# Performance work log

Measured on AMD Instinct MI355X. Metric: run time of the kernel, lower is better.

The kernel has to match this reference:

```python
import jax, jax.numpy as jnp
import numpy as np

N = 100000   # nodes
E = 1600000  # edges
IN, HID, OUT = 128, 128, 64


def setup_inputs() -> dict:
    key = jax.random.key(0)
    ks = jax.random.split(key, 8)
    x = jax.random.normal(ks[0], (N, IN), dtype=jnp.float32)
    edge_index = jax.random.randint(ks[1], (2, E), 0, N, dtype=jnp.int64)
    W1 = jax.random.normal(ks[2], (IN, HID), dtype=jnp.float32) * 0.05
    b1 = jnp.zeros((HID,), dtype=jnp.float32)
    W2 = jax.random.normal(ks[3], (HID, OUT), dtype=jnp.float32) * 0.05
    b2 = jnp.zeros((OUT,), dtype=jnp.float32)
    Wd = jax.random.normal(ks[4], (OUT, IN), dtype=jnp.float32) * 0.05
    bd = jnp.zeros((IN,), dtype=jnp.float32)
    return {"x": x, "edge_index": edge_index, "W1": W1, "b1": b1,
            "W2": W2, "b2": b2, "Wd": Wd, "bd": bd}


def _gcn_conv(x, src, dst, W, b):
    # PyG GCNConv: add self-loops, symmetric normalization D^-1/2 (A+I) D^-1/2,
    # messages flow src -> dst, aggregated by sum at dst.
    h = x @ W                                   # [N, F]
    ones = jnp.ones((src.shape[0],), x.dtype)
    deg = jax.ops.segment_sum(ones, dst, num_segments=N) + 1.0  # +1 for self-loop
    dinv = jax.lax.rsqrt(deg)                   # deg^-1/2, [N]
    coef = dinv[src] * dinv[dst]                # per-edge norm
    agg = jax.ops.segment_sum(h[src] * coef[:, None], dst, num_segments=N)
    agg = agg + h * (dinv * dinv)[:, None]      # self-loop contribution
    return agg + b


def reference(x, edge_index, W1, b1, W2, b2, Wd, bd):
    src, dst = edge_index[0], edge_index[1]
    h = jax.nn.relu(_gcn_conv(x, src, dst, W1, b1))
    # dropout in eval mode -> identity
    z = _gcn_conv(h, src, dst, W2, b2)          # [N, OUT] embedding
    x_recon = z @ Wd + bd                        # [N, IN]
    return (x_recon, z)
```

## Files before the change

### kernel.cpp

```cpp
#include <hip/hip_runtime.h>
#include <hip/hip_bf16.h>
#include <hip/hip_fp16.h>


#define TPB 256
#define CAP 64

typedef float v2f __attribute__((ext_vector_type(2)));


__device__ __forceinline__ unsigned short f2bf(float f) {
    unsigned u = __float_as_uint(f);
    unsigned r = u + 0x7fffu + ((u >> 16) & 1u);
    return (unsigned short)(r >> 16);
}
__device__ __forceinline__ float bf_lo(unsigned u) { return __uint_as_float(u << 16); }
__device__ __forceinline__ float bf_hi(unsigned u) { return __uint_as_float(u & 0xffff0000u); }


__global__ void count_k(const int* __restrict__ dst, int* __restrict__ cnt, int E) {
    int e0 = (blockIdx.x * TPB + threadIdx.x) * 4;
    if (e0 + 3 < E) {
        int4 d4 = *(const int4*)&dst[e0];
        atomicAdd(&cnt[d4.x], 1);
        atomicAdd(&cnt[d4.y], 1);
        atomicAdd(&cnt[d4.z], 1);
        atomicAdd(&cnt[d4.w], 1);
    } else {
        for (int e = e0; e < E; ++e) atomicAdd(&cnt[dst[e]], 1);
    }
}

__global__ void prep_k(const int* __restrict__ cnt, float* __restrict__ dinv,
                       int* __restrict__ cursor, int N) {
    int i = blockIdx.x * TPB + threadIdx.x;
    if (i < N) {
        dinv[i]   = rsqrtf((float)cnt[i] + 1.0f);
        cursor[i] = 0;
    }
}

__global__ void fill_k(const int* __restrict__ src, const int* __restrict__ dst,
                       int* __restrict__ cursor, const float* __restrict__ dinv,
                       unsigned* __restrict__ bucket, int E) {
    int e0 = (blockIdx.x * TPB + threadIdx.x) * 4;
    if (e0 + 3 < E) {
        int4 s4 = *(const int4*)&src[e0];
        int4 d4 = *(const int4*)&dst[e0];
        int ss[4] = {s4.x, s4.y, s4.z, s4.w};
        int dd[4] = {d4.x, d4.y, d4.z, d4.w};
#pragma unroll
        for (int q = 0; q < 4; ++q) {
            float c = dinv[ss[q]] * dinv[dd[q]];
            unsigned short hb = __half_as_ushort(__float2half(c));
            unsigned entry = ((unsigned)ss[q] << 15) | (unsigned)hb;
            int r = atomicAdd(&cursor[dd[q]], 1);
            if (r < CAP) bucket[(size_t)dd[q] * CAP + r] = entry;
        }
    } else {
        for (int e = e0; e < E; ++e) {
            int s = src[e], d = dst[e];
            float c = dinv[s] * dinv[d];
            unsigned short hb = __half_as_ushort(__float2half(c));
            unsigned entry = ((unsigned)s << 15) | (unsigned)hb;
            int r = atomicAdd(&cursor[d], 1);
            if (r < CAP) bucket[(size_t)d * CAP + r] = entry;
        }
    }
}


template <int K, int C, int TN, bool BIAS, bool INBF, bool OUTBF>
__global__ __launch_bounds__(TPB) void gemm_k(const void* __restrict__ Ap,
                                              const float* __restrict__ W,
                                              const float* __restrict__ bias,
                                              void* __restrict__ outp, int N) {
    constexpr int BM  = 128;
    constexpr int TM  = 8;
    constexpr int NCT = C / TN;
    static_assert(NCT * (BM / TM) == TPB, "thread layout");

    __shared__ float Ws[K * C];
    int tid = threadIdx.x;
    for (int i = tid * 4; i < K * C; i += TPB * 4)
        *(float4*)&Ws[i] = *(const float4*)&W[i];
    __syncthreads();

    int tc = tid % NCT;
    int tr = tid / NCT;
    int c0 = tc * TN;
    int r0 = blockIdx.x * BM + tr * TM;

    float acc[TM][TN] = {};

    for (int k = 0; k < K; k += 4) {
        float4 a[TM];
        uint2  au[TM];
#pragma unroll
        for (int i = 0; i < TM; ++i) {
            int r = r0 + i;
            if (r >= N) r = N - 1;
            if (INBF)
                au[i] = *(const uint2*)((const unsigned short*)Ap + (size_t)r * K + k);
            else
                a[i] = *(const float4*)((const float*)Ap + (size_t)r * K + k);
        }
#pragma unroll
        for (int kk = 0; kk < 4; ++kk) {
            float w[TN];
#pragma unroll
            for (int j = 0; j < TN; j += 4)
                *(float4*)&w[j] = *(const float4*)&Ws[(k + kk) * C + c0 + j];
#pragma unroll
            for (int i = 0; i < TM; ++i) {
                float av;
                if (INBF) {
                    unsigned uu = (kk < 2) ? au[i].x : au[i].y;
                    av = (kk & 1) ? bf_hi(uu) : bf_lo(uu);
                } else {
                    av = ((const float*)&a[i])[kk];
                }
#pragma unroll
                for (int j = 0; j < TN; ++j) acc[i][j] += av * w[j];
            }
        }
    }

#pragma unroll
    for (int i = 0; i < TM; ++i) {
        int r = r0 + i;
        if (r >= N) continue;
        if (BIAS) {
#pragma unroll
            for (int j = 0; j < TN; ++j) acc[i][j] += bias[c0 + j];
        }
        if (OUTBF) {
            unsigned short* ob = (unsigned short*)outp + (size_t)r * C + c0;
            unsigned pk[TN / 2];
#pragma unroll
            for (int j = 0; j < TN; j += 2)
                pk[j / 2] = (unsigned)f2bf(acc[i][j]) | ((unsigned)f2bf(acc[i][j + 1]) << 16);
            if (TN == 8)      *(uint4*)ob = *(uint4*)pk;
            else if (TN == 4) *(uint2*)ob = *(uint2*)pk;
        } else {
            float* of = (float*)outp + (size_t)r * C + c0;
#pragma unroll
            for (int j = 0; j < TN; j += 4)
                *(float4*)&of[j] = *(float4*)&acc[i][j];
        }
    }
}


template <int F2, bool RELU, bool OUTBF>
__global__ __launch_bounds__(TPB) void agg_k(const unsigned* __restrict__ h,
                                             const int* __restrict__ cnt,
                                             const unsigned* __restrict__ bucket,
                                             const float* __restrict__ dinv,
                                             const float* __restrict__ bias,
                                             void* __restrict__ outp, int N) {
    constexpr int NPB = TPB / F2;
    int ln = threadIdx.x / F2;
    int f2 = threadIdx.x % F2;
    int n  = blockIdx.x * NPB + ln;
    if (n >= N) return;

    float di = dinv[n];
    unsigned us = h[(size_t)n * F2 + f2];
    float ax = bf_lo(us) * (di * di);
    float ay = bf_hi(us) * (di * di);

    int cn = cnt[n];
    if (cn > CAP) cn = CAP;
    const unsigned* bk = bucket + (size_t)n * CAP;

    int j = 0;
    for (; j + 7 < cn; j += 8) {
        unsigned e[8], v[8];
        float c[8];
#pragma unroll
        for (int q = 0; q < 8; ++q) e[q] = bk[j + q];
#pragma unroll
        for (int q = 0; q < 8; ++q) {
            int s = (int)(e[q] >> 15);
            v[q] = h[(size_t)s * F2 + f2];
            c[q] = __half2float(__ushort_as_half((unsigned short)(e[q] & 0x7fffu)));
        }
#pragma unroll
        for (int q = 0; q < 8; ++q) {
            ax += c[q] * bf_lo(v[q]);
            ay += c[q] * bf_hi(v[q]);
        }
    }
    for (; j < cn; ++j) {
        unsigned e = bk[j];
        int s = (int)(e >> 15);
        unsigned v = h[(size_t)s * F2 + f2];
        float c = __half2float(__ushort_as_half((unsigned short)(e & 0x7fffu)));
        ax += c * bf_lo(v);
        ay += c * bf_hi(v);
    }

    float rx = ax + bias[2 * f2];
    float ry = ay + bias[2 * f2 + 1];
    if (RELU) { rx = fmaxf(rx, 0.f); ry = fmaxf(ry, 0.f); }
    if (OUTBF) {
        unsigned pk = (unsigned)f2bf(rx) | ((unsigned)f2bf(ry) << 16);
        ((unsigned*)outp)[(size_t)n * F2 + f2] = pk;
    } else {
        v2f r; r.x = rx; r.y = ry;
        __builtin_nontemporal_store(r, (v2f*)outp + (size_t)n * F2 + f2);
    }
}


extern "C" void kernel_launch(void* const* d_in, const int* in_sizes, int n_in,
                              void* d_out, int out_size, void* d_ws, size_t ws_size,
                              hipStream_t stream) {
    const float* x    = (const float*)d_in[0];
    const int*   eidx = (const int*)d_in[1];
    const float* W1   = (const float*)d_in[2];
    const float* b1   = (const float*)d_in[3];
    const float* W2   = (const float*)d_in[4];
    const float* b2   = (const float*)d_in[5];
    const float* Wd   = (const float*)d_in[6];
    const float* bd   = (const float*)d_in[7];

    const int N = in_sizes[0] / 128;
    const int E = in_sizes[1] / 2;
    const int* src = eidx;
    const int* dst = eidx + E;

    size_t off = 0;
    auto alloc = [&](size_t bytes) {
        void* p = (char*)d_ws + off;
        off += (bytes + 255) & ~(size_t)255;
        return p;
    };
    int*      cnt      = (int*)alloc((size_t)N * 4);
    int*      cursor   = (int*)alloc((size_t)N * 4);
    float*    dinv     = (float*)alloc((size_t)N * 4);
    unsigned* bucket   = (unsigned*)alloc((size_t)N * CAP * 4);
    unsigned* h1b      = (unsigned*)alloc((size_t)N * 64 * 4);
    unsigned* h2b      = (unsigned*)alloc((size_t)N * 32 * 4);
    unsigned* hrelu_b  = (unsigned*)alloc((size_t)N * 64 * 4);
    (void)ws_size;

    float* x_recon = (float*)d_out;
    float* z_out   = (float*)d_out + (size_t)N * 128;

    const int eb4 = (E / 4 + TPB - 1) / TPB;
    const int nb  = (N + TPB - 1) / TPB;
    const int gb  = (N + 127) / 128;

    (void)hipMemsetAsync(cnt, 0, (size_t)N * 4, stream);
    count_k<<<eb4, TPB, 0, stream>>>(dst, cnt, E);
    prep_k<<<nb, TPB, 0, stream>>>(cnt, dinv, cursor, N);
    fill_k<<<eb4, TPB, 0, stream>>>(src, dst, cursor, dinv, bucket, E);

    gemm_k<128, 128, 8, false, false, true><<<gb, TPB, 0, stream>>>(x, W1, nullptr, h1b, N);
    agg_k<64, true, true><<<(N + 3) / 4, TPB, 0, stream>>>(h1b, cnt, bucket, dinv, b1,
                                                           hrelu_b, N);
    gemm_k<128, 64, 4, false, true, true><<<gb, TPB, 0, stream>>>(hrelu_b, W2, nullptr, h2b, N);
    agg_k<32, false, false><<<(N + 7) / 8, TPB, 0, stream>>>(h2b, cnt, bucket, dinv, b2,
                                                             z_out, N);
    gemm_k<64, 128, 8, true, false, false><<<gb, TPB, 0, stream>>>(z_out, Wd, bd, x_recon, N);
}
```

Before: 546.9 us.

## Merge graph build into single atomic pass fused with first GEMM, compute norms on the fly

Replaces the separate count, prep and fill kernels with one pass where the atomic counter doubles as the bucket cursor, and runs that pass in the same launch as the first GEMM using extra blocks. Buckets now hold only source indices, and per-edge normalisation is recomputed in the aggregation kernels from cnt via rsqrt, which removes the dinv array and one full edge pass. GEMM weights are staged in 32-row K-tiles to shrink shared memory so the fused blocks can co-reside. The cost is an extra random cnt gather per edge in both aggregations and more barriers in the GEMM.

New measurement: 479.2 us. 12.4% less time.

```diff
diff --git a/kernel.cpp b/kernel.cpp
--- a/kernel.cpp
+++ b/kernel.cpp
@@ -18,110 +18,62 @@
 __device__ __forceinline__ float bf_hi(unsigned u) { return __uint_as_float(u & 0xffff0000u); }
 
 
-__global__ void count_k(const int* __restrict__ dst, int* __restrict__ cnt, int E) {
-    int e0 = (blockIdx.x * TPB + threadIdx.x) * 4;
-    if (e0 + 3 < E) {
-        int4 d4 = *(const int4*)&dst[e0];
-        atomicAdd(&cnt[d4.x], 1);
-        atomicAdd(&cnt[d4.y], 1);
-        atomicAdd(&cnt[d4.z], 1);
-        atomicAdd(&cnt[d4.w], 1);
-    } else {
-        for (int e = e0; e < E; ++e) atomicAdd(&cnt[dst[e]], 1);
-    }
-}
-
-__global__ void prep_k(const int* __restrict__ cnt, float* __restrict__ dinv,
-                       int* __restrict__ cursor, int N) {
-    int i = blockIdx.x * TPB + threadIdx.x;
-    if (i < N) {
-        dinv[i]   = rsqrtf((float)cnt[i] + 1.0f);
-        cursor[i] = 0;
-    }
-}
-
-__global__ void fill_k(const int* __restrict__ src, const int* __restrict__ dst,
-                       int* __restrict__ cursor, const float* __restrict__ dinv,
-                       unsigned* __restrict__ bucket, int E) {
-    int e0 = (blockIdx.x * TPB + threadIdx.x) * 4;
-    if (e0 + 3 < E) {
-        int4 s4 = *(const int4*)&src[e0];
-        int4 d4 = *(const int4*)&dst[e0];
-        int ss[4] = {s4.x, s4.y, s4.z, s4.w};
-        int dd[4] = {d4.x, d4.y, d4.z, d4.w};
-#pragma unroll
-        for (int q = 0; q < 4; ++q) {
-            float c = dinv[ss[q]] * dinv[dd[q]];
-            unsigned short hb = __half_as_ushort(__float2half(c));
-            unsigned entry = ((unsigned)ss[q] << 15) | (unsigned)hb;
-            int r = atomicAdd(&cursor[dd[q]], 1);
-            if (r < CAP) bucket[(size_t)dd[q] * CAP + r] = entry;
-        }
-    } else {
-        for (int e = e0; e < E; ++e) {
-            int s = src[e], d = dst[e];
-            float c = dinv[s] * dinv[d];
-            unsigned short hb = __half_as_ushort(__float2half(c));
-            unsigned entry = ((unsigned)s << 15) | (unsigned)hb;
-            int r = atomicAdd(&cursor[d], 1);
-            if (r < CAP) bucket[(size_t)d * CAP + r] = entry;
-        }
-    }
-}
-
-
 template <int K, int C, int TN, bool BIAS, bool INBF, bool OUTBF>
-__global__ __launch_bounds__(TPB) void gemm_k(const void* __restrict__ Ap,
-                                              const float* __restrict__ W,
-                                              const float* __restrict__ bias,
-                                              void* __restrict__ outp, int N) {
+__device__ __forceinline__ void gemm_body(const void* __restrict__ Ap,
+                                          const float* __restrict__ W,
+                                          const float* __restrict__ bias,
+                                          void* __restrict__ outp, int N, int bid,
+                                          float* __restrict__ Ws) {
     constexpr int BM  = 128;
     constexpr int TM  = 8;
+    constexpr int BK  = 32;
     constexpr int NCT = C / TN;
     static_assert(NCT * (BM / TM) == TPB, "thread layout");
 
-    __shared__ float Ws[K * C];
     int tid = threadIdx.x;
-    for (int i = tid * 4; i < K * C; i += TPB * 4)
-        *(float4*)&Ws[i] = *(const float4*)&W[i];
-    __syncthreads();
-
     int tc = tid % NCT;
     int tr = tid / NCT;
     int c0 = tc * TN;
-    int r0 = blockIdx.x * BM + tr * TM;
+    int r0 = bid * BM + tr * TM;
 
     float acc[TM][TN] = {};
 
-    for (int k = 0; k < K; k += 4) {
-        float4 a[TM];
-        uint2  au[TM];
-#pragma unroll
-        for (int i = 0; i < TM; ++i) {
-            int r = r0 + i;
-            if (r >= N) r = N - 1;
-            if (INBF)
-                au[i] = *(const uint2*)((const unsigned short*)Ap + (size_t)r * K + k);
-            else
-                a[i] = *(const float4*)((const float*)Ap + (size_t)r * K + k);
-        }
-#pragma unroll
-        for (int kk = 0; kk < 4; ++kk) {
-            float w[TN];
-#pragma unroll
-            for (int j = 0; j < TN; j += 4)
-                *(float4*)&w[j] = *(const float4*)&Ws[(k + kk) * C + c0 + j];
+    for (int k0 = 0; k0 < K; k0 += BK) {
+        __syncthreads();
+        for (int i = tid * 4; i < BK * C; i += TPB * 4)
+            *(float4*)&Ws[i] = *(const float4*)&W[k0 * C + i];
+        __syncthreads();
+
+        for (int k = 0; k < BK; k += 4) {
+            float4 a[TM];
+            uint2  au[TM];
 #pragma unroll
             for (int i = 0; i < TM; ++i) {
-                float av;
-                if (INBF) {
-                    unsigned uu = (kk < 2) ? au[i].x : au[i].y;
-                    av = (kk & 1) ? bf_hi(uu) : bf_lo(uu);
-                } else {
-                    av = ((const float*)&a[i])[kk];
+                int r = r0 + i;
+                if (r >= N) r = N - 1;
+                if (INBF)
+                    au[i] = *(const uint2*)((const unsigned short*)Ap + (size_t)r * K + k0 + k);
+                else
+                    a[i] = *(const float4*)((const float*)Ap + (size_t)r * K + k0 + k);
+            }
+#pragma unroll
+            for (int kk = 0; kk < 4; ++kk) {
+                float w[TN];
+#pragma unroll
+                for (int j = 0; j < TN; j += 4)
+                    *(float4*)&w[j] = *(const float4*)&Ws[(k + kk) * C + c0 + j];
+#pragma unroll
+                for (int i = 0; i < TM; ++i) {
+                    float av;
+                    if (INBF) {
+                        unsigned uu = (kk < 2) ? au[i].x : au[i].y;
+                        av = (kk & 1) ? bf_hi(uu) : bf_lo(uu);
+                    } else {
+                        av = ((const float*)&a[i])[kk];
+                    }
+#pragma unroll
+                    for (int j = 0; j < TN; ++j) acc[i][j] += av * w[j];
                 }
-#pragma unroll
-                for (int j = 0; j < TN; ++j) acc[i][j] += av * w[j];
             }
         }
     }
@@ -151,12 +103,58 @@
     }
 }
 
+template <int K, int C, int TN, bool BIAS, bool INBF, bool OUTBF>
+__global__ __launch_bounds__(TPB) void gemm_k(const void* __restrict__ Ap,
+                                              const float* __restrict__ W,
+                                              const float* __restrict__ bias,
+                                              void* __restrict__ outp, int N) {
+    __shared__ float Ws[32 * C];
+    gemm_body<K, C, TN, BIAS, INBF, OUTBF>(Ap, W, bias, outp, N, blockIdx.x, Ws);
+}
+
+
+__global__ __launch_bounds__(TPB) void fused1_k(const float* __restrict__ x,
+                                                const float* __restrict__ W1,
+                                                unsigned* __restrict__ h1b,
+                                                const int* __restrict__ src,
+                                                const int* __restrict__ dst,
+                                                int* __restrict__ cnt,
+                                                unsigned* __restrict__ bucket,
+                                                int N, int E, int gb) {
+    __shared__ float Ws[32 * 128];
+    if ((int)blockIdx.x < gb) {
+        gemm_body<128, 128, 8, false, false, true>(x, W1, nullptr, h1b, N, blockIdx.x, Ws);
+    } else {
+        int bid = (int)blockIdx.x - gb;
+        int e0 = (bid * TPB + (int)threadIdx.x) * 8;
+        if (e0 + 7 < E) {
+            int4 sa = *(const int4*)&src[e0];
+            int4 sb = *(const int4*)&src[e0 + 4];
+            int4 da = *(const int4*)&dst[e0];
+            int4 db = *(const int4*)&dst[e0 + 4];
+            int ss[8] = {sa.x, sa.y, sa.z, sa.w, sb.x, sb.y, sb.z, sb.w};
+            int dd[8] = {da.x, da.y, da.z, da.w, db.x, db.y, db.z, db.w};
+            int rr[8];
+#pragma unroll
+            for (int q = 0; q < 8; ++q) rr[q] = atomicAdd(&cnt[dd[q]], 1);
+#pragma unroll
+            for (int q = 0; q < 8; ++q)
+                if (rr[q] < CAP) bucket[(size_t)dd[q] * CAP + rr[q]] = (unsigned)ss[q];
+        } else {
+            for (int e = e0; e < E; ++e) {
+                int s = src[e], d = dst[e];
+                int r = atomicAdd(&cnt[d], 1);
+                if (r < CAP) bucket[(size_t)d * CAP + r] = (unsigned)s;
+            }
+        }
+    }
+}
+
 
 template <int F2, bool RELU, bool OUTBF>
 __global__ __launch_bounds__(TPB) void agg_k(const unsigned* __restrict__ h,
                                              const int* __restrict__ cnt,
                                              const unsigned* __restrict__ bucket,
-                                             const float* __restrict__ dinv,
                                              const float* __restrict__ bias,
                                              void* __restrict__ outp, int N) {
     constexpr int NPB = TPB / F2;
@@ -165,38 +163,37 @@
     int n  = blockIdx.x * NPB + ln;
     if (n >= N) return;
 
-    float di = dinv[n];
+    int cfull = cnt[n];
+    float di = rsqrtf((float)cfull + 1.0f);
     unsigned us = h[(size_t)n * F2 + f2];
     float ax = bf_lo(us) * (di * di);
     float ay = bf_hi(us) * (di * di);
 
-    int cn = cnt[n];
-    if (cn > CAP) cn = CAP;
+    int cn = cfull < CAP ? cfull : CAP;
     const unsigned* bk = bucket + (size_t)n * CAP;
 
     int j = 0;
     for (; j + 7 < cn; j += 8) {
-        unsigned e[8], v[8];
-        float c[8];
-#pragma unroll
-        for (int q = 0; q < 8; ++q) e[q] = bk[j + q];
+        int s[8], cs[8];
+        unsigned v[8];
+#pragma unroll
+        for (int q = 0; q < 8; ++q) s[q] = (int)bk[j + q];
 #pragma unroll
         for (int q = 0; q < 8; ++q) {
-            int s = (int)(e[q] >> 15);
-            v[q] = h[(size_t)s * F2 + f2];
-            c[q] = __half2float(__ushort_as_half((unsigned short)(e[q] & 0x7fffu)));
+            v[q]  = h[(size_t)s[q] * F2 + f2];
+            cs[q] = cnt[s[q]];
         }
 #pragma unroll
         for (int q = 0; q < 8; ++q) {
-            ax += c[q] * bf_lo(v[q]);
-            ay += c[q] * bf_hi(v[q]);
+            float c = rsqrtf((float)cs[q] + 1.0f) * di;
+            ax += c * bf_lo(v[q]);
+            ay += c * bf_hi(v[q]);
         }
     }
     for (; j < cn; ++j) {
-        unsigned e = bk[j];
-        int s = (int)(e >> 15);
+        int s = (int)bk[j];
         unsigned v = h[(size_t)s * F2 + f2];
-        float c = __half2float(__ushort_as_half((unsigned short)(e & 0x7fffu)));
+        float c = rsqrtf((float)cnt[s] + 1.0f) * di;
         ax += c * bf_lo(v);
         ay += c * bf_hi(v);
     }
@@ -237,32 +234,25 @@
         off += (bytes + 255) & ~(size_t)255;
         return p;
     };
-    int*      cnt      = (int*)alloc((size_t)N * 4);
-    int*      cursor   = (int*)alloc((size_t)N * 4);
-    float*    dinv     = (float*)alloc((size_t)N * 4);
-    unsigned* bucket   = (unsigned*)alloc((size_t)N * CAP * 4);
-    unsigned* h1b      = (unsigned*)alloc((size_t)N * 64 * 4);
-    unsigned* h2b      = (unsigned*)alloc((size_t)N * 32 * 4);
-    unsigned* hrelu_b  = (unsigned*)alloc((size_t)N * 64 * 4);
+    int*      cnt     = (int*)alloc((size_t)N * 4);
+    unsigned* bucket  = (unsigned*)alloc((size_t)N * CAP * 4);
+    unsigned* h1b     = (unsigned*)alloc((size_t)N * 64 * 4);
+    unsigned* h2b     = (unsigned*)alloc((size_t)N * 32 * 4);
+    unsigned* hrelu_b = (unsigned*)alloc((size_t)N * 64 * 4);
     (void)ws_size;
 
     float* x_recon = (float*)d_out;
     float* z_out   = (float*)d_out + (size_t)N * 128;
 
-    const int eb4 = (E / 4 + TPB - 1) / TPB;
-    const int nb  = (N + TPB - 1) / TPB;
-    const int gb  = (N + 127) / 128;
+    const int gb = (N + 127) / 128;
+    const int fb = (E + TPB * 8 - 1) / (TPB * 8);
 
     (void)hipMemsetAsync(cnt, 0, (size_t)N * 4, stream);
-    count_k<<<eb4, TPB, 0, stream>>>(dst, cnt, E);
-    prep_k<<<nb, TPB, 0, stream>>>(cnt, dinv, cursor, N);
-    fill_k<<<eb4, TPB, 0, stream>>>(src, dst, cursor, dinv, bucket, E);
-
-    gemm_k<128, 128, 8, false, false, true><<<gb, TPB, 0, stream>>>(x, W1, nullptr, h1b, N);
-    agg_k<64, true, true><<<(N + 3) / 4, TPB, 0, stream>>>(h1b, cnt, bucket, dinv, b1,
-                                                           hrelu_b, N);
+
+    fused1_k<<<gb + fb, TPB, 0, stream>>>(x, W1, h1b, src, dst, cnt, bucket, N, E, gb);
+
+    agg_k<64, true, true><<<(N + 3) / 4, TPB, 0, stream>>>(h1b, cnt, bucket, b1, hrelu_b, N);
     gemm_k<128, 64, 4, false, true, true><<<gb, TPB, 0, stream>>>(hrelu_b, W2, nullptr, h2b, N);
-    agg_k<32, false, false><<<(N + 7) / 8, TPB, 0, stream>>>(h2b, cnt, bucket, dinv, b2,
-                                                             z_out, N);
+    agg_k<32, false, false><<<(N + 7) / 8, TPB, 0, stream>>>(h2b, cnt, bucket, b2, z_out, N);
     gemm_k<64, 128, 8, true, false, false><<<gb, TPB, 0, stream>>>(z_out, Wd, bd, x_recon, N);
 }
```
